# Kernel optimization log

Measured on AMD Instinct MI355X. Metric: run time of the kernel, lower is better.

The kernel has to match this reference:

```python
import jax, jax.numpy as jnp
import numpy as np
import math

E = 256      # emb_size
H = 4        # num_heads
D = E // H   # head_dim
EXPLORE_SCALE = 0.5
EXPLOIT_SCALE = 0.5
TEMP_MIN = 0.5
TEMP_MAX = 2.0


def setup_inputs() -> dict:
    key = jax.random.key(0)
    ks = jax.random.split(key, 12)
    B, S = 4, 2048
    his_emb = jax.random.normal(ks[0], (B, S, E), dtype=jnp.float32)
    src_key_padding_mask = jax.random.randint(ks[1], (B, S), 0, 2) > 0
    explore = jax.random.uniform(ks[2], (B, S), dtype=jnp.float32)
    exploit = jax.random.uniform(ks[3], (B, S), dtype=jnp.float32)
    scale = 1.0 / math.sqrt(E)
    Wq = jax.random.normal(ks[4], (E, E), dtype=jnp.float32) * scale
    bq = jnp.zeros((E,), dtype=jnp.float32)
    Wk = jax.random.normal(ks[5], (E, E), dtype=jnp.float32) * scale
    bk = jnp.zeros((E,), dtype=jnp.float32)
    Wv = jax.random.normal(ks[6], (E, E), dtype=jnp.float32) * scale
    bv = jnp.zeros((E,), dtype=jnp.float32)
    Wo = jax.random.normal(ks[7], (E, E), dtype=jnp.float32) * scale
    bo = jnp.zeros((E,), dtype=jnp.float32)
    return {"his_emb": his_emb, "src_key_padding_mask": src_key_padding_mask,
            "explore": explore, "exploit": exploit,
            "Wq": Wq, "bq": bq, "Wk": Wk, "bk": bk,
            "Wv": Wv, "bv": bv, "Wo": Wo, "bo": bo}


def reference(his_emb, src_key_padding_mask, explore, exploit,
              Wq, bq, Wk, bk, Wv, bv, Wo, bo):
    B, S, _ = his_emb.shape
    # projections -> [B, H, S, D]
    q = (his_emb @ Wq + bq).reshape(B, S, H, D).transpose(0, 2, 1, 3)
    k = (his_emb @ Wk + bk).reshape(B, S, H, D).transpose(0, 2, 1, 3)
    v = (his_emb @ Wv + bv).reshape(B, S, H, D).transpose(0, 2, 1, 3)
    logits = jnp.einsum('bhqd,bhkd->bhqk', q, k) / math.sqrt(D)
    attn_mask = src_key_padding_mask[:, None, None, :]  # [B,1,1,S] over keys
    logits = jnp.where(attn_mask, -1e16, logits)
    # per-query dynamic temperature
    temp = 1.0 + EXPLORE_SCALE * explore - EXPLOIT_SCALE * exploit  # [B,S]
    temp = jnp.clip(temp, TEMP_MIN, TEMP_MAX)
    temp = jnp.where(src_key_padding_mask, 1.0, temp)
    logits = logits / temp[:, None, :, None]
    probs = jax.nn.softmax(logits, axis=-1)
    probs = jnp.where(attn_mask, 0.0, probs)
    probs = probs / jnp.maximum(probs.sum(axis=-1, keepdims=True), 1e-8)
    out = jnp.einsum('bhqk,bhkd->bhqd', probs, v)
    out = out.transpose(0, 2, 1, 3).reshape(B, S, E)
    out = out @ Wo + bo
    return jnp.where(src_key_padding_mask[:, :, None], 0.0, out)
```

## Files before the change

kernel.cpp:

```cpp
#include <hip/hip_runtime.h>
#include <hip/hip_bf16.h>
#include <math.h>

#define B_ 4
#define S_ 2048
#define E_ 256
#define H_ 4
#define D_ 64
#define NROW (B_*S_)
#define NCH 2
#define CHK (S_/NCH)
#define FM 12.0f

typedef __attribute__((ext_vector_type(8))) short short8;
typedef __attribute__((ext_vector_type(4))) float floatx4;

__device__ __forceinline__ short f2bf(float f){
    union{float f; unsigned u;} x; x.f = f;
    unsigned r = x.u + 0x7fffu + ((x.u>>16)&1u);
    return (short)(r>>16);
}

__global__ __launch_bounds__(256) void transpose_w(
    const float* __restrict__ W0, const float* __restrict__ W1,
    const float* __restrict__ W2, const float* __restrict__ W3,
    short* __restrict__ T0, short* __restrict__ T1,
    short* __restrict__ T2, short* __restrict__ T3)
{
    const float* W = blockIdx.y==0?W0: blockIdx.y==1?W1: blockIdx.y==2?W2:W3;
    short*       T = blockIdx.y==0?T0: blockIdx.y==1?T1: blockIdx.y==2?T2:T3;
    __shared__ float L[64][65];
    const int t = threadIdx.x;
    const int k0 = (blockIdx.x>>2)*64, n0 = (blockIdx.x&3)*64;
    {
        int r = t>>2, c0 = (t&3)*16;
        const float4* p = (const float4*)(W + (size_t)(k0+r)*E_ + n0 + c0);
        #pragma unroll
        for (int j=0;j<4;++j){
            float4 u = p[j];
            L[r][c0+4*j]=u.x; L[r][c0+4*j+1]=u.y; L[r][c0+4*j+2]=u.z; L[r][c0+4*j+3]=u.w;
        }
    }
    __syncthreads();
    {
        int n = t>>2, kk0 = (t&3)*16;
        short8 o0, o1;
        #pragma unroll
        for(int j=0;j<8;++j) o0[j] = f2bf(L[kk0+j][n]);
        #pragma unroll
        for(int j=0;j<8;++j) o1[j] = f2bf(L[kk0+8+j][n]);
        short* dst = T + (size_t)(n0+n)*E_ + k0 + kk0;
        *(short8*)dst = o0; *(short8*)(dst+8) = o1;
    }
}

__global__ __launch_bounds__(256) void qkv_gemm(
    const float* __restrict__ X,
    const short* __restrict__ Wtq, const float* __restrict__ bq,
    const short* __restrict__ Wtk, const float* __restrict__ bk,
    const short* __restrict__ Wtv, const float* __restrict__ bv,
    short* __restrict__ Q, short* __restrict__ K, short* __restrict__ Vt)
{
    const int z = blockIdx.z;
    const short* Wt   = z==0?Wtq: z==1?Wtk:Wtv;
    const float* bias = z==0?bq:  z==1?bk:bv;

    __shared__ __align__(16) short As[64][72];
    __shared__ __align__(16) short Bs[64][72];

    const int t=threadIdx.x, w=t>>6, lane=t&63, ln=lane&15, quad=lane>>4;
    const int m0 = blockIdx.y*64, n0 = blockIdx.x*64;

    floatx4 acc[4] = {};
    for (int kt=0; kt<E_; kt+=64){
        __syncthreads();
        {
            int r=t>>2, c0=(t&3)*16;
            const float4* pa = (const float4*)(X + (size_t)(m0+r)*E_ + kt + c0);
            short8 s0, s1;
            float4 u;
            u=pa[0]; s0[0]=f2bf(u.x); s0[1]=f2bf(u.y); s0[2]=f2bf(u.z); s0[3]=f2bf(u.w);
            u=pa[1]; s0[4]=f2bf(u.x); s0[5]=f2bf(u.y); s0[6]=f2bf(u.z); s0[7]=f2bf(u.w);
            u=pa[2]; s1[0]=f2bf(u.x); s1[1]=f2bf(u.y); s1[2]=f2bf(u.z); s1[3]=f2bf(u.w);
            u=pa[3]; s1[4]=f2bf(u.x); s1[5]=f2bf(u.y); s1[6]=f2bf(u.z); s1[7]=f2bf(u.w);
            *(short8*)&As[r][c0] = s0; *(short8*)&As[r][c0+8] = s1;
            const uint4* pb = (const uint4*)(Wt + (size_t)(n0+r)*E_ + kt + c0);
            *(uint4*)&Bs[r][c0] = pb[0]; *(uint4*)&Bs[r][c0+8] = pb[1];
        }
        __syncthreads();
        short8 a0 = *(const short8*)&As[w*16+ln][quad*8];
        short8 a1 = *(const short8*)&As[w*16+ln][32+quad*8];
        #pragma unroll
        for (int c=0;c<4;++c){
            short8 b0 = *(const short8*)&Bs[c*16+ln][quad*8];
            short8 b1 = *(const short8*)&Bs[c*16+ln][32+quad*8];
            acc[c] = __builtin_amdgcn_mfma_f32_16x16x32_bf16(a0,b0,acc[c],0,0,0);
            acc[c] = __builtin_amdgcn_mfma_f32_16x16x32_bf16(a1,b1,acc[c],0,0,0);
        }
    }
    if (z<2){
        short* dst = z==0?Q:K;
        #pragma unroll
        for(int c=0;c<4;++c){
            int colg = n0 + c*16 + ln;
            float bia = bias[colg];
            #pragma unroll
            for(int reg=0;reg<4;++reg){
                int row = m0 + w*16 + quad*4 + reg;
                dst[(size_t)row*E_ + colg] = f2bf(acc[c][reg] + bia);
            }
        }
    } else {
        #pragma unroll
        for(int c=0;c<4;++c){
            int colg = n0 + c*16 + ln;
            int hx = colg>>6, d = colg&63;
            float bia = bias[colg];
            #pragma unroll
            for(int reg=0;reg<4;++reg){
                int row = m0 + w*16 + quad*4 + reg;
                int bb = row>>11, s = row&(S_-1);
                Vt[((size_t)((bb*H_+hx)*D_+d))*S_ + s] = f2bf(acc[c][reg] + bia);
            }
        }
    }
}

__global__ __launch_bounds__(256) void attn_mfma(
    const short* __restrict__ Qb, const short* __restrict__ Kb, const short* __restrict__ Vtb,
    const int* __restrict__ mask,
    const float* __restrict__ explore, const float* __restrict__ exploit,
    float* __restrict__ OP, float* __restrict__ Lb)
{
    const int z = blockIdx.z;
    const int b = z>>2, h = z&3;
    const int q0 = blockIdx.x*64;
    const int ck = blockIdx.y;
    const int k0 = ck*CHK;
    const int t=threadIdx.x, w=t>>6, lane=t&63, ln=lane&15, quad=lane>>4;

    __shared__ __align__(16) short Ks[64][72];
    __shared__ __align__(16) short Vs[64][72];
    __shared__ __align__(16) short Ps[4][16][72];
    __shared__ float mb[64];

    float tsc[4], lacc[4];
    #pragma unroll
    for (int reg=0; reg<4; ++reg){
        int qg = q0 + w*16 + quad*4 + reg;
        float ex = explore[b*S_+qg], xp = exploit[b*S_+qg];
        float tmp = fminf(fmaxf(1.0f + 0.5f*ex - 0.5f*xp, 0.5f), 2.0f);
        if (mask[b*S_+qg]) tmp = 1.0f;
        tsc[reg]  = 1.0f/(tmp*8.0f);
        lacc[reg] = 0.0f;
    }
    const size_t qrow = (size_t)(b*S_ + q0 + w*16 + ln)*E_ + h*D_;
    short8 qa0 = *(const short8*)(Qb + qrow + quad*8);
    short8 qa1 = *(const short8*)(Qb + qrow + 32 + quad*8);

    floatx4 of[4] = {};

    for (int kt=k0; kt<k0+CHK; kt+=64){
        __syncthreads();
        {
            int r=t>>2, c0=(t&3)*16;
            const uint4* gk = (const uint4*)(Kb + (size_t)(b*S_+kt+r)*E_ + h*D_ + c0);
            *(uint4*)&Ks[r][c0] = gk[0]; *(uint4*)&Ks[r][c0+8] = gk[1];
            const uint4* gv = (const uint4*)(Vtb + ((size_t)((b*H_+h)*D_+r))*S_ + kt + c0);
            *(uint4*)&Vs[r][c0] = gv[0]; *(uint4*)&Vs[r][c0+8] = gv[1];
        }
        if (t<64) mb[t] = mask[b*S_+kt+t] ? -1e30f : 0.0f;
        __syncthreads();

        floatx4 sf[4];
        #pragma unroll
        for (int c=0;c<4;++c){
            short8 kb0 = *(const short8*)&Ks[c*16+ln][quad*8];
            short8 kb1 = *(const short8*)&Ks[c*16+ln][32+quad*8];
            floatx4 zz = {};
            zz = __builtin_amdgcn_mfma_f32_16x16x32_bf16(qa0,kb0,zz,0,0,0);
            zz = __builtin_amdgcn_mfma_f32_16x16x32_bf16(qa1,kb1,zz,0,0,0);
            sf[c] = zz;
        }

        float mbc[4];
        #pragma unroll
        for(int c=0;c<4;++c) mbc[c] = mb[c*16+ln];

        #pragma unroll
        for(int reg=0;reg<4;++reg){
            #pragma unroll
            for(int c=0;c<4;++c){
                float p = __expf(sf[c][reg]*tsc[reg] + mbc[c] - FM);
                Ps[w][quad*4+reg][c*16+ln] = f2bf(p);
                lacc[reg] += p;
            }
        }

        short8 pa0 = *(const short8*)&Ps[w][ln][quad*8];
        short8 pa1 = *(const short8*)&Ps[w][ln][32+quad*8];
        #pragma unroll
        for(int dc=0;dc<4;++dc){
            short8 vb0 = *(const short8*)&Vs[dc*16+ln][quad*8];
            short8 vb1 = *(const short8*)&Vs[dc*16+ln][32+quad*8];
            of[dc] = __builtin_amdgcn_mfma_f32_16x16x32_bf16(pa0,vb0,of[dc],0,0,0);
            of[dc] = __builtin_amdgcn_mfma_f32_16x16x32_bf16(pa1,vb1,of[dc],0,0,0);
        }
    }

    #pragma unroll
    for(int reg=0;reg<4;++reg){
        float l = lacc[reg];
        l += __shfl_xor(l,1); l += __shfl_xor(l,2);
        l += __shfl_xor(l,4); l += __shfl_xor(l,8);
        int qg = q0 + w*16 + quad*4 + reg;
        float* dst = OP + (((size_t)(ck*B_+b)*H_+h)*S_ + qg)*D_;
        #pragma unroll
        for(int dc=0;dc<4;++dc) dst[dc*16+ln] = of[dc][reg];
        if (ln==0) Lb[((size_t)(ck*B_+b)*H_+h)*S_ + qg] = l;
    }
}

__global__ __launch_bounds__(256) void combine(
    const float* __restrict__ OP, const float* __restrict__ Lb, short* __restrict__ CTXb)
{
    int gid = blockIdx.x*256 + threadIdx.x;
    #pragma unroll
    for (int i=0;i<4;++i){
        int idx = gid + i*524288;
        int e = idx & 255, row = idx >> 8;
        int bb = row >> 11, s = row & (S_-1);
        int hh = e >> 6, d = e & 63;
        float o = 0.f, l = 0.f;
        #pragma unroll
        for (int c=0;c<NCH;++c){
            o += OP[(((size_t)(c*B_+bb)*H_+hh)*S_+s)*D_ + d];
            l += Lb[((size_t)(c*B_+bb)*H_+hh)*S_+s];
        }
        CTXb[idx] = f2bf(o / fmaxf(l, 1e-8f));
    }
}

__global__ __launch_bounds__(256) void out_gemm(
    const short* __restrict__ Ab, const short* __restrict__ Wto, const float* __restrict__ bo,
    const int* __restrict__ mask, float* __restrict__ out)
{
    __shared__ __align__(16) short As[64][72];
    __shared__ __align__(16) short Bs[64][72];
    const int t=threadIdx.x, w=t>>6, lane=t&63, ln=lane&15, quad=lane>>4;
    const int m0 = blockIdx.y*64, n0 = blockIdx.x*64;
    floatx4 acc[4] = {};
    for (int kt=0; kt<E_; kt+=64){
        __syncthreads();
        {
            int r=t>>2, c0=(t&3)*16;
            const uint4* pa = (const uint4*)(Ab + (size_t)(m0+r)*E_ + kt + c0);
            *(uint4*)&As[r][c0] = pa[0]; *(uint4*)&As[r][c0+8] = pa[1];
            const uint4* pb = (const uint4*)(Wto + (size_t)(n0+r)*E_ + kt + c0);
            *(uint4*)&Bs[r][c0] = pb[0]; *(uint4*)&Bs[r][c0+8] = pb[1];
        }
        __syncthreads();
        short8 a0 = *(const short8*)&As[w*16+ln][quad*8];
        short8 a1 = *(const short8*)&As[w*16+ln][32+quad*8];
        #pragma unroll
        for (int c=0;c<4;++c){
            short8 b0 = *(const short8*)&Bs[c*16+ln][quad*8];
            short8 b1 = *(const short8*)&Bs[c*16+ln][32+quad*8];
            acc[c] = __builtin_amdgcn_mfma_f32_16x16x32_bf16(a0,b0,acc[c],0,0,0);
            acc[c] = __builtin_amdgcn_mfma_f32_16x16x32_bf16(a1,b1,acc[c],0,0,0);
        }
    }
    #pragma unroll
    for(int c=0;c<4;++c){
        int colg = n0 + c*16 + ln;
        float bia = bo[colg];
        #pragma unroll
        for(int reg=0;reg<4;++reg){
            int row = m0 + w*16 + quad*4 + reg;
            out[(size_t)row*E_ + colg] = mask[row] ? 0.0f : (acc[c][reg] + bia);
        }
    }
}

extern "C" void kernel_launch(void* const* d_in, const int* in_sizes, int n_in,
                              void* d_out, int out_size, void* d_ws, size_t ws_size,
                              hipStream_t stream) {
    const float* his     = (const float*)d_in[0];
    const int*   mask    = (const int*)d_in[1];
    const float* explore = (const float*)d_in[2];
    const float* exploit = (const float*)d_in[3];
    const float* Wq = (const float*)d_in[4];
    const float* bq = (const float*)d_in[5];
    const float* Wk = (const float*)d_in[6];
    const float* bk = (const float*)d_in[7];
    const float* Wv = (const float*)d_in[8];
    const float* bv = (const float*)d_in[9];
    const float* Wo = (const float*)d_in[10];
    const float* bo = (const float*)d_in[11];

    char* ws = (char*)d_ws;
    const size_t NE2 = (size_t)NROW * E_ * 2;
    short* Wtq  = (short*)(ws);                    ws += E_*E_*2;
    short* Wtk  = (short*)(ws);                    ws += E_*E_*2;
    short* Wtv  = (short*)(ws);                    ws += E_*E_*2;
    short* Wto  = (short*)(ws);                    ws += E_*E_*2;
    short* Qb   = (short*)(ws);                    ws += NE2;
    short* Kb   = (short*)(ws);                    ws += NE2;
    short* Vtb  = (short*)(ws);                    ws += NE2;
    float* OP   = (float*)(ws);                    ws += (size_t)NCH*NROW*E_*4;
    float* Lb   = (float*)(ws);                    ws += (size_t)NCH*B_*H_*S_*4;
    short* CTXb = Qb;

    transpose_w<<<dim3(16,4), 256, 0, stream>>>(Wq, Wk, Wv, Wo, Wtq, Wtk, Wtv, Wto);

    qkv_gemm<<<dim3(E_/64, NROW/64, 3), 256, 0, stream>>>(
        his, Wtq, bq, Wtk, bk, Wtv, bv, Qb, Kb, Vtb);

    attn_mfma<<<dim3(S_/64, NCH, B_*H_), 256, 0, stream>>>(
        Qb, Kb, Vtb, mask, explore, exploit, OP, Lb);

    combine<<<2048, 256, 0, stream>>>(OP, Lb, CTXb);

    out_gemm<<<dim3(E_/64, NROW/64), 256, 0, stream>>>(CTXb, Wto, bo, mask, (float*)d_out);
}
```

Baseline: 147.8 us.

## Rewrite attention with 32x32 MFMA, double-buffered K/V, and fused combine into out GEMM

Attention now uses 32x32x16 MFMA tiles with 128 queries per block, computes S^T so probabilities stay in registers and are repacked with cvt_pk and permlane32_swap instead of going through shared memory. K/V tiles are double-buffered with register prefetch, exp2 with a folded log2e scale is used, and blocks are swizzled. The separate combine kernel is removed: out_gemm now sums the two chunk partials, normalizes and converts to bf16 while loading its A tile. The input bf16 conversion moves into the prep kernel. This adds an extra bf16 copy of the input and more register pressure per attention block.

```diff
diff --git a/kernel.cpp b/kernel.cpp
--- a/kernel.cpp
+++ b/kernel.cpp
@@ -1,5 +1,4 @@
 #include <hip/hip_runtime.h>
-#include <hip/hip_bf16.h>
 #include <math.h>
 
 #define B_ 4
@@ -10,27 +9,47 @@
 #define NROW (B_*S_)
 #define NCH 2
 #define CHK (S_/NCH)
-#define FM 12.0f
-
-typedef __attribute__((ext_vector_type(8))) short short8;
-typedef __attribute__((ext_vector_type(4))) float floatx4;
+#define NT (CHK/64)
+#define LOG2E 1.4426950408889634f
+#define NFM  (-17.312340490667562f)
+
+typedef __attribute__((ext_vector_type(8)))  short short8;
+typedef __attribute__((ext_vector_type(4)))  float floatx4;
+typedef __attribute__((ext_vector_type(16))) float floatx16;
 
 __device__ __forceinline__ short f2bf(float f){
     union{float f; unsigned u;} x; x.f = f;
     unsigned r = x.u + 0x7fffu + ((x.u>>16)&1u);
     return (short)(r>>16);
 }
-
-__global__ __launch_bounds__(256) void transpose_w(
+__device__ __forceinline__ unsigned cvtpk(float a, float b){
+    unsigned r; asm("v_cvt_pk_bf16_f32 %0, %1, %2" : "=v"(r) : "v"(a), "v"(b)); return r;
+}
+
+__global__ __launch_bounds__(256) void prep(
     const float* __restrict__ W0, const float* __restrict__ W1,
     const float* __restrict__ W2, const float* __restrict__ W3,
+    const float* __restrict__ X,
     short* __restrict__ T0, short* __restrict__ T1,
-    short* __restrict__ T2, short* __restrict__ T3)
+    short* __restrict__ T2, short* __restrict__ T3,
+    short* __restrict__ Xb)
 {
+    __shared__ float L[64][65];
+    const int t = threadIdx.x;
+    if (blockIdx.x >= 16){
+        const int cid = (blockIdx.x - 16) + 128*blockIdx.y;
+        const float4* src = (const float4*)(X + (size_t)cid*4096 + t*16);
+        short8 o0, o1; float4 u;
+        u = src[0]; o0[0]=f2bf(u.x); o0[1]=f2bf(u.y); o0[2]=f2bf(u.z); o0[3]=f2bf(u.w);
+        u = src[1]; o0[4]=f2bf(u.x); o0[5]=f2bf(u.y); o0[6]=f2bf(u.z); o0[7]=f2bf(u.w);
+        u = src[2]; o1[0]=f2bf(u.x); o1[1]=f2bf(u.y); o1[2]=f2bf(u.z); o1[3]=f2bf(u.w);
+        u = src[3]; o1[4]=f2bf(u.x); o1[5]=f2bf(u.y); o1[6]=f2bf(u.z); o1[7]=f2bf(u.w);
+        short* dst = Xb + (size_t)cid*4096 + t*16;
+        *(short8*)dst = o0; *(short8*)(dst+8) = o1;
+        return;
+    }
     const float* W = blockIdx.y==0?W0: blockIdx.y==1?W1: blockIdx.y==2?W2:W3;
     short*       T = blockIdx.y==0?T0: blockIdx.y==1?T1: blockIdx.y==2?T2:T3;
-    __shared__ float L[64][65];
-    const int t = threadIdx.x;
     const int k0 = (blockIdx.x>>2)*64, n0 = (blockIdx.x&3)*64;
     {
         int r = t>>2, c0 = (t&3)*16;
@@ -55,7 +74,7 @@
 }
 
 __global__ __launch_bounds__(256) void qkv_gemm(
-    const float* __restrict__ X,
+    const short* __restrict__ Xb,
     const short* __restrict__ Wtq, const float* __restrict__ bq,
     const short* __restrict__ Wtk, const float* __restrict__ bk,
     const short* __restrict__ Wtv, const float* __restrict__ bv,
@@ -76,14 +95,8 @@
         __syncthreads();
         {
             int r=t>>2, c0=(t&3)*16;
-            const float4* pa = (const float4*)(X + (size_t)(m0+r)*E_ + kt + c0);
-            short8 s0, s1;
-            float4 u;
-            u=pa[0]; s0[0]=f2bf(u.x); s0[1]=f2bf(u.y); s0[2]=f2bf(u.z); s0[3]=f2bf(u.w);
-            u=pa[1]; s0[4]=f2bf(u.x); s0[5]=f2bf(u.y); s0[6]=f2bf(u.z); s0[7]=f2bf(u.w);
-            u=pa[2]; s1[0]=f2bf(u.x); s1[1]=f2bf(u.y); s1[2]=f2bf(u.z); s1[3]=f2bf(u.w);
-            u=pa[3]; s1[4]=f2bf(u.x); s1[5]=f2bf(u.y); s1[6]=f2bf(u.z); s1[7]=f2bf(u.w);
-            *(short8*)&As[r][c0] = s0; *(short8*)&As[r][c0+8] = s1;
+            const uint4* pa = (const uint4*)(Xb + (size_t)(m0+r)*E_ + kt + c0);
+            *(uint4*)&As[r][c0] = pa[0]; *(uint4*)&As[r][c0+8] = pa[1];
             const uint4* pb = (const uint4*)(Wt + (size_t)(n0+r)*E_ + kt + c0);
             *(uint4*)&Bs[r][c0] = pb[0]; *(uint4*)&Bs[r][c0+8] = pb[1];
         }
@@ -132,151 +145,201 @@
     const float* __restrict__ explore, const float* __restrict__ exploit,
     float* __restrict__ OP, float* __restrict__ Lb)
 {
-    const int z = blockIdx.z;
-    const int b = z>>2, h = z&3;
-    const int q0 = blockIdx.x*64;
-    const int ck = blockIdx.y;
+    const int bid = blockIdx.x + 16*blockIdx.y + 32*blockIdx.z;
+    const int swz = (bid & 7)*64 + (bid >> 3);
+    const int bx = swz & 15;
+    const int ck = (swz >> 4) & 1;
+    const int z  = swz >> 5;
+    const int b = z >> 2, h = z & 3;
+    const int q0 = bx*128;
     const int k0 = ck*CHK;
-    const int t=threadIdx.x, w=t>>6, lane=t&63, ln=lane&15, quad=lane>>4;
-
-    __shared__ __align__(16) short Ks[64][72];
-    __shared__ __align__(16) short Vs[64][72];
-    __shared__ __align__(16) short Ps[4][16][72];
-    __shared__ float mb[64];
-
-    float tsc[4], lacc[4];
-    #pragma unroll
-    for (int reg=0; reg<4; ++reg){
-        int qg = q0 + w*16 + quad*4 + reg;
+
+    const int t = threadIdx.x, w = t>>6, lane = t&63, l31 = lane&31, hi = lane>>5;
+
+    __shared__ __align__(16) short Ks[2][64][72];
+    __shared__ __align__(16) short Vs[2][64][72];
+    __shared__ float mb[2][64];
+
+    const int qbase = q0 + w*32;
+    const int qg = qbase + l31;
+    float tsc2;
+    {
         float ex = explore[b*S_+qg], xp = exploit[b*S_+qg];
         float tmp = fminf(fmaxf(1.0f + 0.5f*ex - 0.5f*xp, 0.5f), 2.0f);
         if (mask[b*S_+qg]) tmp = 1.0f;
-        tsc[reg]  = 1.0f/(tmp*8.0f);
-        lacc[reg] = 0.0f;
-    }
-    const size_t qrow = (size_t)(b*S_ + q0 + w*16 + ln)*E_ + h*D_;
-    short8 qa0 = *(const short8*)(Qb + qrow + quad*8);
-    short8 qa1 = *(const short8*)(Qb + qrow + 32 + quad*8);
-
-    floatx4 of[4] = {};
-
-    for (int kt=k0; kt<k0+CHK; kt+=64){
-        __syncthreads();
-        {
-            int r=t>>2, c0=(t&3)*16;
-            const uint4* gk = (const uint4*)(Kb + (size_t)(b*S_+kt+r)*E_ + h*D_ + c0);
-            *(uint4*)&Ks[r][c0] = gk[0]; *(uint4*)&Ks[r][c0+8] = gk[1];
-            const uint4* gv = (const uint4*)(Vtb + ((size_t)((b*H_+h)*D_+r))*S_ + kt + c0);
-            *(uint4*)&Vs[r][c0] = gv[0]; *(uint4*)&Vs[r][c0+8] = gv[1];
-        }
-        if (t<64) mb[t] = mask[b*S_+kt+t] ? -1e30f : 0.0f;
-        __syncthreads();
-
-        floatx4 sf[4];
-        #pragma unroll
-        for (int c=0;c<4;++c){
-            short8 kb0 = *(const short8*)&Ks[c*16+ln][quad*8];
-            short8 kb1 = *(const short8*)&Ks[c*16+ln][32+quad*8];
-            floatx4 zz = {};
-            zz = __builtin_amdgcn_mfma_f32_16x16x32_bf16(qa0,kb0,zz,0,0,0);
-            zz = __builtin_amdgcn_mfma_f32_16x16x32_bf16(qa1,kb1,zz,0,0,0);
-            sf[c] = zz;
-        }
-
-        float mbc[4];
-        #pragma unroll
-        for(int c=0;c<4;++c) mbc[c] = mb[c*16+ln];
-
-        #pragma unroll
-        for(int reg=0;reg<4;++reg){
+        tsc2 = LOG2E/(tmp*8.0f);
+    }
+    const size_t qrow = (size_t)(b*S_+qg)*E_ + h*D_ + hi*8;
+    const short8 qf0 = *(const short8*)(Qb + qrow);
+    const short8 qf1 = *(const short8*)(Qb + qrow + 16);
+    const short8 qf2 = *(const short8*)(Qb + qrow + 32);
+    const short8 qf3 = *(const short8*)(Qb + qrow + 48);
+
+    floatx16 ofa = {}, ofb = {};
+    float lacc = 0.0f;
+
+    const int sr = t>>2, sc = (t&3)*16;
+    const short* kgp = Kb  + (size_t)(b*S_)*E_ + h*D_ + sc;
+    const short* vgp = Vtb + ((size_t)(b*H_+h)*D_ + sr)*S_;
+
+    uint4 rk0, rk1, rv0, rv1; float mfv = 0.0f;
+    {
+        const uint4* gk = (const uint4*)(kgp + (size_t)(k0+sr)*E_);
+        rk0 = gk[0]; rk1 = gk[1];
+        const uint4* gv = (const uint4*)(vgp + k0 + sc);
+        rv0 = gv[0]; rv1 = gv[1];
+        if (t < 64) mfv = mask[b*S_ + k0 + t] ? -1e30f : NFM;
+    }
+    *(uint4*)&Ks[0][sr][sc] = rk0; *(uint4*)&Ks[0][sr][sc+8] = rk1;
+    *(uint4*)&Vs[0][sr][sc] = rv0; *(uint4*)&Vs[0][sr][sc+8] = rv1;
+    if (t < 64) mb[0][t] = mfv;
+    {
+        const uint4* gk = (const uint4*)(kgp + (size_t)(k0+64+sr)*E_);
+        rk0 = gk[0]; rk1 = gk[1];
+        const uint4* gv = (const uint4*)(vgp + k0 + 64 + sc);
+        rv0 = gv[0]; rv1 = gv[1];
+        if (t < 64) mfv = mask[b*S_ + k0 + 64 + t] ? -1e30f : NFM;
+    }
+    __syncthreads();
+
+    int cur = 0;
+    #pragma unroll 1
+    for (int it = 0; it < NT; ++it){
+        const short (*Kc)[72] = Ks[cur];
+        const short (*Vc)[72] = Vs[cur];
+        #pragma unroll
+        for (int kg = 0; kg < 2; ++kg){
+            floatx16 st = {};
+            const short8 kf0 = *(const short8*)&Kc[kg*32+l31][hi*8];
+            const short8 kf1 = *(const short8*)&Kc[kg*32+l31][16+hi*8];
+            const short8 kf2 = *(const short8*)&Kc[kg*32+l31][32+hi*8];
+            const short8 kf3 = *(const short8*)&Kc[kg*32+l31][48+hi*8];
+            __builtin_amdgcn_s_setprio(1);
+            st = __builtin_amdgcn_mfma_f32_32x32x16_bf16(kf0, qf0, st, 0,0,0);
+            st = __builtin_amdgcn_mfma_f32_32x32x16_bf16(kf1, qf1, st, 0,0,0);
+            st = __builtin_amdgcn_mfma_f32_32x32x16_bf16(kf2, qf2, st, 0,0,0);
+            st = __builtin_amdgcn_mfma_f32_32x32x16_bf16(kf3, qf3, st, 0,0,0);
+            __builtin_amdgcn_s_setprio(0);
+            const float4 m0_ = *(const float4*)&mb[cur][kg*32 +      4*hi];
+            const float4 m1_ = *(const float4*)&mb[cur][kg*32 +  8 + 4*hi];
+            const float4 m2_ = *(const float4*)&mb[cur][kg*32 + 16 + 4*hi];
+            const float4 m3_ = *(const float4*)&mb[cur][kg*32 + 24 + 4*hi];
+            const float mbf[16] = {m0_.x,m0_.y,m0_.z,m0_.w, m1_.x,m1_.y,m1_.z,m1_.w,
+                                   m2_.x,m2_.y,m2_.z,m2_.w, m3_.x,m3_.y,m3_.z,m3_.w};
+            float p[16];
             #pragma unroll
-            for(int c=0;c<4;++c){
-                float p = __expf(sf[c][reg]*tsc[reg] + mbc[c] - FM);
-                Ps[w][quad*4+reg][c*16+ln] = f2bf(p);
-                lacc[reg] += p;
-            }
-        }
-
-        short8 pa0 = *(const short8*)&Ps[w][ln][quad*8];
-        short8 pa1 = *(const short8*)&Ps[w][ln][32+quad*8];
-        #pragma unroll
-        for(int dc=0;dc<4;++dc){
-            short8 vb0 = *(const short8*)&Vs[dc*16+ln][quad*8];
-            short8 vb1 = *(const short8*)&Vs[dc*16+ln][32+quad*8];
-            of[dc] = __builtin_amdgcn_mfma_f32_16x16x32_bf16(pa0,vb0,of[dc],0,0,0);
-            of[dc] = __builtin_amdgcn_mfma_f32_16x16x32_bf16(pa1,vb1,of[dc],0,0,0);
-        }
-    }
-
+            for (int r = 0; r < 16; ++r){
+                p[r] = __builtin_amdgcn_exp2f(st[r]*tsc2 + mbf[r]);
+                lacc += p[r];
+            }
+            #pragma unroll
+            for (int c = 0; c < 2; ++c){
+                unsigned w0 = cvtpk(p[c*8+0], p[c*8+1]);
+                unsigned w1 = cvtpk(p[c*8+2], p[c*8+3]);
+                unsigned w2 = cvtpk(p[c*8+4], p[c*8+5]);
+                unsigned w3 = cvtpk(p[c*8+6], p[c*8+7]);
+                asm("v_permlane32_swap_b32 %0, %1" : "+v"(w0), "+v"(w2));
+                asm("v_permlane32_swap_b32 %0, %1" : "+v"(w1), "+v"(w3));
+                union { uint4 u; short8 s; } pc;
+                pc.u.x = w0; pc.u.y = w1; pc.u.z = w2; pc.u.w = w3;
+                const short8 vf0 = *(const short8*)&Vc[l31]   [kg*32 + c*16 + hi*8];
+                const short8 vf1 = *(const short8*)&Vc[32+l31][kg*32 + c*16 + hi*8];
+                __builtin_amdgcn_s_setprio(1);
+                ofa = __builtin_amdgcn_mfma_f32_32x32x16_bf16(pc.s, vf0, ofa, 0,0,0);
+                ofb = __builtin_amdgcn_mfma_f32_32x32x16_bf16(pc.s, vf1, ofb, 0,0,0);
+                __builtin_amdgcn_s_setprio(0);
+            }
+        }
+        if (it + 1 < NT){
+            *(uint4*)&Ks[cur^1][sr][sc] = rk0; *(uint4*)&Ks[cur^1][sr][sc+8] = rk1;
+            *(uint4*)&Vs[cur^1][sr][sc] = rv0; *(uint4*)&Vs[cur^1][sr][sc+8] = rv1;
+            if (t < 64) mb[cur^1][t] = mfv;
+            if (it + 2 < NT){
+                const int kt2 = k0 + (it+2)*64;
+                const uint4* gk = (const uint4*)(kgp + (size_t)(kt2+sr)*E_);
+                rk0 = gk[0]; rk1 = gk[1];
+                const uint4* gv = (const uint4*)(vgp + kt2 + sc);
+                rv0 = gv[0]; rv1 = gv[1];
+                if (t < 64) mfv = mask[b*S_ + kt2 + t] ? -1e30f : NFM;
+            }
+        }
+        __syncthreads();
+        cur ^= 1;
+    }
+
+    const float l = lacc + __shfl_xor(lacc, 32);
+    const size_t obase = ((size_t)(ck*B_+b)*H_+h)*S_;
+    if (hi == 0) Lb[obase + qg] = l;
     #pragma unroll
-    for(int reg=0;reg<4;++reg){
-        float l = lacc[reg];
-        l += __shfl_xor(l,1); l += __shfl_xor(l,2);
-        l += __shfl_xor(l,4); l += __shfl_xor(l,8);
-        int qg = q0 + w*16 + quad*4 + reg;
-        float* dst = OP + (((size_t)(ck*B_+b)*H_+h)*S_ + qg)*D_;
-        #pragma unroll
-        for(int dc=0;dc<4;++dc) dst[dc*16+ln] = of[dc][reg];
-        if (ln==0) Lb[((size_t)(ck*B_+b)*H_+h)*S_ + qg] = l;
-    }
-}
-
-__global__ __launch_bounds__(256) void combine(
-    const float* __restrict__ OP, const float* __restrict__ Lb, short* __restrict__ CTXb)
-{
-    int gid = blockIdx.x*256 + threadIdx.x;
-    #pragma unroll
-    for (int i=0;i<4;++i){
-        int idx = gid + i*524288;
-        int e = idx & 255, row = idx >> 8;
-        int bb = row >> 11, s = row & (S_-1);
-        int hh = e >> 6, d = e & 63;
-        float o = 0.f, l = 0.f;
-        #pragma unroll
-        for (int c=0;c<NCH;++c){
-            o += OP[(((size_t)(c*B_+bb)*H_+hh)*S_+s)*D_ + d];
-            l += Lb[((size_t)(c*B_+bb)*H_+hh)*S_+s];
-        }
-        CTXb[idx] = f2bf(o / fmaxf(l, 1e-8f));
+    for (int r = 0; r < 16; ++r){
+        const int q = qbase + (r&3) + 8*(r>>2) + 4*hi;
+        float* dst = OP + (obase + q)*D_;
+        dst[l31]      = ofa[r];
+        dst[32 + l31] = ofb[r];
     }
 }
 
 __global__ __launch_bounds__(256) void out_gemm(
-    const short* __restrict__ Ab, const short* __restrict__ Wto, const float* __restrict__ bo,
+    const float* __restrict__ OP, const float* __restrict__ Lb,
+    const short* __restrict__ Wto, const float* __restrict__ bo,
     const int* __restrict__ mask, float* __restrict__ out)
 {
     __shared__ __align__(16) short As[64][72];
     __shared__ __align__(16) short Bs[64][72];
+    const int bid = blockIdx.x + 4*blockIdx.y;
+    const int swz = (bid & 7)*64 + (bid >> 3);
+    const int n0 = (swz & 3)*64;
+    const int m0 = (swz >> 2)*64;
     const int t=threadIdx.x, w=t>>6, lane=t&63, ln=lane&15, quad=lane>>4;
-    const int m0 = blockIdx.y*64, n0 = blockIdx.x*64;
     floatx4 acc[4] = {};
+    const int sr=t>>2, sc=(t&3)*16;
+    const int rowg = m0 + sr, bb = rowg>>11, ss = rowg&(S_-1);
+    #pragma unroll 1
     for (int kt=0; kt<E_; kt+=64){
-        __syncthreads();
-        {
-            int r=t>>2, c0=(t&3)*16;
-            const uint4* pa = (const uint4*)(Ab + (size_t)(m0+r)*E_ + kt + c0);
-            *(uint4*)&As[r][c0] = pa[0]; *(uint4*)&As[r][c0+8] = pa[1];
-            const uint4* pb = (const uint4*)(Wto + (size_t)(n0+r)*E_ + kt + c0);
-            *(uint4*)&Bs[r][c0] = pb[0]; *(uint4*)&Bs[r][c0+8] = pb[1];
-        }
-        __syncthreads();
-        short8 a0 = *(const short8*)&As[w*16+ln][quad*8];
-        short8 a1 = *(const short8*)&As[w*16+ln][32+quad*8];
+        const int hx = kt>>6;
+        const size_t r0 = ((size_t)(bb)*H_+hx)*S_+ss;
+        const size_t r1 = ((size_t)(B_+bb)*H_+hx)*S_+ss;
+        const float lsum = Lb[r0] + Lb[r1];
+        const float rl = 1.0f/fmaxf(lsum, 1e-8f);
+        const float* pa0 = OP + r0*D_ + sc;
+        const float* pa1 = OP + r1*D_ + sc;
+        const float4 u0 = *(const float4*)(pa0+0), u1 = *(const float4*)(pa0+4),
+                     u2 = *(const float4*)(pa0+8), u3 = *(const float4*)(pa0+12);
+        const float4 v0 = *(const float4*)(pa1+0), v1 = *(const float4*)(pa1+4),
+                     v2 = *(const float4*)(pa1+8), v3 = *(const float4*)(pa1+12);
+        const uint4* pb = (const uint4*)(Wto + (size_t)(n0+sr)*E_ + kt + sc);
+        const uint4 bw0 = pb[0], bw1 = pb[1];
+        __syncthreads();
+        union { uint4 u; short8 s; } cA, cB;
+        cA.u.x = cvtpk((u0.x+v0.x)*rl, (u0.y+v0.y)*rl);
+        cA.u.y = cvtpk((u0.z+v0.z)*rl, (u0.w+v0.w)*rl);
+        cA.u.z = cvtpk((u1.x+v1.x)*rl, (u1.y+v1.y)*rl);
+        cA.u.w = cvtpk((u1.z+v1.z)*rl, (u1.w+v1.w)*rl);
+        cB.u.x = cvtpk((u2.x+v2.x)*rl, (u2.y+v2.y)*rl);
+        cB.u.y = cvtpk((u2.z+v2.z)*rl, (u2.w+v2.w)*rl);
+        cB.u.z = cvtpk((u3.x+v3.x)*rl, (u3.y+v3.y)*rl);
+        cB.u.w = cvtpk((u3.z+v3.z)*rl, (u3.w+v3.w)*rl);
+        *(short8*)&As[sr][sc]   = cA.s;
+        *(short8*)&As[sr][sc+8] = cB.s;
+        *(uint4*)&Bs[sr][sc] = bw0; *(uint4*)&Bs[sr][sc+8] = bw1;
+        __syncthreads();
+        const short8 a0 = *(const short8*)&As[w*16+ln][quad*8];
+        const short8 a1 = *(const short8*)&As[w*16+ln][32+quad*8];
         #pragma unroll
         for (int c=0;c<4;++c){
-            short8 b0 = *(const short8*)&Bs[c*16+ln][quad*8];
-            short8 b1 = *(const short8*)&Bs[c*16+ln][32+quad*8];
+            const short8 b0 = *(const short8*)&Bs[c*16+ln][quad*8];
+            const short8 b1 = *(const short8*)&Bs[c*16+ln][32+quad*8];
             acc[c] = __builtin_amdgcn_mfma_f32_16x16x32_bf16(a0,b0,acc[c],0,0,0);
             acc[c] = __builtin_amdgcn_mfma_f32_16x16x32_bf16(a1,b1,acc[c],0,0,0);
         }
     }
     #pragma unroll
     for(int c=0;c<4;++c){
-        int colg = n0 + c*16 + ln;
-        float bia = bo[colg];
+        const int colg = n0 + c*16 + ln;
+        const float bia = bo[colg];
         #pragma unroll
         for(int reg=0;reg<4;++reg){
-            int row = m0 + w*16 + quad*4 + reg;
+            const int row = m0 + w*16 + quad*4 + reg;
             out[(size_t)row*E_ + colg] = mask[row] ? 0.0f : (acc[c][reg] + bia);
         }
     }
@@ -304,22 +367,20 @@
     short* Wtk  = (short*)(ws);                    ws += E_*E_*2;
     short* Wtv  = (short*)(ws);                    ws += E_*E_*2;
     short* Wto  = (short*)(ws);                    ws += E_*E_*2;
+    short* Xb   = (short*)(ws);                    ws += NE2;
     short* Qb   = (short*)(ws);                    ws += NE2;
     short* Kb   = (short*)(ws);                    ws += NE2;
     short* Vtb  = (short*)(ws);                    ws += NE2;
     float* OP   = (float*)(ws);                    ws += (size_t)NCH*NROW*E_*4;
     float* Lb   = (float*)(ws);                    ws += (size_t)NCH*B_*H_*S_*4;
-    short* CTXb = Qb;
-
-    transpose_w<<<dim3(16,4), 256, 0, stream>>>(Wq, Wk, Wv, Wo, Wtq, Wtk, Wtv, Wto);
+
+    prep<<<dim3(144,4), 256, 0, stream>>>(Wq, Wk, Wv, Wo, his, Wtq, Wtk, Wtv, Wto, Xb);
 
     qkv_gemm<<<dim3(E_/64, NROW/64, 3), 256, 0, stream>>>(
-        his, Wtq, bq, Wtk, bk, Wtv, bv, Qb, Kb, Vtb);
-
-    attn_mfma<<<dim3(S_/64, NCH, B_*H_), 256, 0, stream>>>(
+        Xb, Wtq, bq, Wtk, bk, Wtv, bv, Qb, Kb, Vtb);
+
+    attn_mfma<<<dim3(S_/128, NCH, B_*H_), 256, 0, stream>>>(
         Qb, Kb, Vtb, mask, explore, exploit, OP, Lb);
 
-    combine<<<2048, 256, 0, stream>>>(OP, Lb, CTXb);
-
-    out_gemm<<<dim3(E_/64, NROW/64), 256, 0, stream>>>(CTXb, Wto, bo, mask, (float*)d_out);
-}
+    out_gemm<<<dim3(E_/64, NROW/64), 256, 0, stream>>>(OP, Lb, Wto, bo, mask, (float*)d_out);
+}
```

Result: faster. 132.2 us (-10.5%).
